# Optimization experiments

Measured on AMD Instinct MI355X. Metric: run time of the kernel, lower is better.

## Reference

```python
import jax, jax.numpy as jnp
import numpy as np

K, D = 512, 256
NUM_CLASSES, SHARED_KEYS = 10, 10
B, H, W = 32, 64, 64
TRAINING = True


def setup_inputs() -> dict:
    key = jax.random.key(0)
    k1, k2, k3 = jax.random.split(key, 3)
    z_e_x = jax.random.normal(k1, (B, D, H, W), dtype=jnp.float32)
    labels = jax.random.randint(k2, (B,), 0, NUM_CLASSES)
    # nn.Embedding weight initialized uniform(-1/K, 1/K)
    codebook = jax.random.uniform(k3, (K, D), minval=-1.0 / K, maxval=1.0 / K,
                                  dtype=jnp.float32)
    return {"z_e_x": z_e_x, "codebook": codebook, "labels": labels}


def _irrelevant_regions(labels_flat, k, num_classes, n_shared, training):
    # uniform partition of the first K - n_shared codes over the classes
    uniform = jnp.round(jnp.linspace(-0.5, num_classes - 0.51, k - n_shared))  # [K-Ns]
    irrel = uniform[None, :] != labels_flat[:, None].astype(uniform.dtype)     # [N, K-Ns]
    n = labels_flat.shape[0]
    if training:
        tail = jnp.ones((n, n_shared), dtype=bool)   # TRAIN: shared keys masked out
    else:
        tail = jnp.zeros((n, n_shared), dtype=bool)
    return jnp.concatenate([irrel, tail], axis=1)    # [N, K]


def reference(z_e_x, codebook, labels):
    x = jnp.transpose(z_e_x, (0, 2, 3, 1))           # [B,H,W,D]
    xf = x.reshape(-1, D)                            # [N,D], N=B*H*W
    labels_flat = jnp.repeat(labels, H * W)          # [N]

    irrel = _irrelevant_regions(labels_flat, K, NUM_CLASSES, SHARED_KEYS, TRAINING)

    cb_sqr = jnp.sum(codebook * codebook, axis=1)                      # [K]
    in_sqr = jnp.sum(xf * xf, axis=1, keepdims=True)                   # [N,1]
    distances = in_sqr + cb_sqr[None, :] - 2.0 * (xf @ codebook.T)     # [N,K]
    distances = jnp.where(irrel, jnp.inf, distances)

    idx = jnp.argmin(distances, axis=1)                                # [N]

    codes = codebook[idx].reshape(x.shape)                             # [B,H,W,D]
    # straight-through path (detached codebook in torch)
    z_q = x + jax.lax.stop_gradient(codes - x)
    z_q_x = jnp.transpose(z_q, (0, 3, 1, 2))                           # [B,D,H,W]
    # non-detached codebook lookup path
    z_q_bar = codebook[jax.lax.stop_gradient(idx)].reshape(x.shape)
    z_q_x_bar = jnp.transpose(z_q_bar, (0, 3, 1, 2))                   # [B,D,H,W]
    return (z_q_x, z_q_x_bar)
```

## Files before the change

### kernel.cpp

```cpp
#include <hip/hip_runtime.h>


#define D       256
#define KCODES  512
#define HW      4096
#define BATCH   32
#define NPTS    (BATCH * HW)
#define WPW     13
#define PF      8

typedef float fx4 __attribute__((ext_vector_type(4)));

__constant__ int c_cls_start[11] = {0, 51, 101, 151, 201, 251, 301, 352, 402, 452, 502};

__global__ __launch_bounds__(256) void prep_kernel(const float* __restrict__ cb,
                                                   float* __restrict__ cbT,
                                                   float* __restrict__ cbs) {
    const int k = blockIdx.x;
    const int d = threadIdx.x;
    float v = cb[k * D + d];
    cbT[(size_t)d * KCODES + k] = v;
    __shared__ double red[256];
    red[d] = (double)v * (double)v;
    __syncthreads();
    for (int s = 128; s > 0; s >>= 1) {
        if (d < s) red[d] += red[d + s];
        __syncthreads();
    }
    if (d == 0) cbs[k] = (float)red[0];
}

__global__ __launch_bounds__(256, 8) void argmin_kernel(const float* __restrict__ z,
                                                        const int* __restrict__ labels,
                                                        const float* __restrict__ cbT,
                                                        const float* __restrict__ cbs,
                                                        int* __restrict__ fidxg) {
    const int lane = threadIdx.x & 63;
    const int w    = __builtin_amdgcn_readfirstlane(threadIdx.x >> 6);
    const int b    = blockIdx.x >> 6;
    const int hw   = ((blockIdx.x & 63) << 6) | lane;
    const int lab  = __builtin_amdgcn_readfirstlane(labels[b]);
    const int c0   = c_cls_start[lab];
    const int cnt  = c_cls_start[lab + 1] - c0;
    const int kbase = c0 + w * WPW;
    const int myn   = min(WPW, cnt - w * WPW);

    const float* __restrict__ xp = z + (size_t)b * (D * HW) + hw;

    float acc[WPW];
#pragma unroll
    for (int j = 0; j < WPW; ++j) acc[j] = 0.0f;

    double xsq = 0.0;

    float xb[PF];
#pragma unroll
    for (int i = 0; i < PF; ++i) xb[i] = xp[(size_t)i * HW];

    for (int d = 0; d < D; d += PF) {
        float xn[PF];
#pragma unroll
        for (int i = 0; i < PF; ++i) {
            int dn = (d + PF + i) & (D - 1);
            xn[i] = xp[(size_t)dn * HW];
        }
#pragma unroll
        for (int i = 0; i < PF; ++i) {
            const float* __restrict__ wd = cbT + (size_t)(d + i) * KCODES + kbase;
            const float x = xb[i];
            xsq = fma((double)x, (double)x, xsq);
#pragma unroll
            for (int j = 0; j < WPW; ++j)
                acc[j] = fmaf(x, wd[j], acc[j]);
        }
#pragma unroll
        for (int i = 0; i < PF; ++i) xb[i] = xn[i];
    }

    const float insq = (float)xsq;
    float best = __builtin_inff();
    int bi = kbase;
#pragma unroll
    for (int j = 0; j < WPW; ++j) {
        if (j < myn) {
            float T    = insq + cbs[kbase + j];
            float dist = fmaf(-2.0f, acc[j], T);
            if (dist < best) { best = dist; bi = kbase + j; }
        }
    }

    __shared__ float sd[4][64];
    __shared__ int   si[4][64];
    sd[w][lane] = best;
    si[w][lane] = bi;
    __syncthreads();
    if (w == 0) {
        float fb = sd[0][lane];
        int   fi = si[0][lane];
#pragma unroll
        for (int w2 = 1; w2 < 4; ++w2) {
            float dv = sd[w2][lane];
            if (dv < fb) { fb = dv; fi = si[w2][lane]; }
        }
        fidxg[(size_t)b * HW + hw] = fi;
    }
}

__global__ __launch_bounds__(256) void emit_kernel(const int* __restrict__ fidxg,
                                                   const float* __restrict__ cbT,
                                                   float* __restrict__ out) {
    const int lane = threadIdx.x & 63;
    const int w    = threadIdx.x >> 6;
    const int s    = blockIdx.x >> 2;
    const int dq   = blockIdx.x & 3;
    const int b    = s >> 4;
    const int p0   = ((s & 15) << 8) | (lane << 2);

    const int4 f = *(const int4*)(fidxg + (size_t)b * HW + p0);

    float* __restrict__ o0 = out + (size_t)b * (D * HW) + p0;
    float* __restrict__ o1 = o0 + (size_t)NPTS * D;
    const int d0 = (dq << 6) | (w << 4);
    const float* __restrict__ row = cbT + (size_t)d0 * KCODES;
#pragma unroll 4
    for (int d = d0; d < d0 + 16; ++d) {
        fx4 v;
        v.x = row[f.x];
        v.y = row[f.y];
        v.z = row[f.z];
        v.w = row[f.w];
        __builtin_nontemporal_store(v, (fx4*)(o0 + (size_t)d * HW));
        __builtin_nontemporal_store(v, (fx4*)(o1 + (size_t)d * HW));
        row += KCODES;
    }
}

extern "C" void kernel_launch(void* const* d_in, const int* in_sizes, int n_in,
                              void* d_out, int out_size, void* d_ws, size_t ws_size,
                              hipStream_t stream) {
    const float* z      = (const float*)d_in[0];
    const float* cb     = (const float*)d_in[1];
    const int*   labels = (const int*)d_in[2];
    float* out = (float*)d_out;

    float* cbT  = (float*)d_ws;
    float* cbs  = cbT + (size_t)D * KCODES;
    int*   fidx = (int*)(cbs + KCODES);

    hipLaunchKernelGGL(prep_kernel, dim3(KCODES), dim3(D), 0, stream, cb, cbT, cbs);
    hipLaunchKernelGGL(argmin_kernel, dim3(NPTS / 64), dim3(256), 0, stream,
                       z, labels, cbT, cbs, fidx);
    hipLaunchKernelGGL(emit_kernel, dim3((NPTS / 256) * 4), dim3(256), 0, stream,
                       fidx, cbT, out);
}
```

Measured before the change: 393.7 us.

## Stage codebook chunks in per-wave double-buffered LDS for the distance loop

The argmin kernel now copies 32-row chunks of the transposed codebook slice for each wave's codes into a per-wave, double-buffered shared-memory tile, using register prefetch two chunks ahead. The inner FMA loop then reads codebook values from LDS instead of issuing wave-uniform global loads. The aim is to hide codebook fetch latency behind compute. The trade-offs are that the previously scalar, constant-cache-friendly uniform loads become LDS broadcast reads, and the kernel now needs 16KB of shared memory per block, which may limit occupancy.

```diff
diff --git a/kernel.cpp b/kernel.cpp
--- a/kernel.cpp
+++ b/kernel.cpp
@@ -8,6 +8,9 @@
 #define NPTS    (BATCH * HW)
 #define WPW     13
 #define PF      8
+#define CHUNK   32
+#define NCH     (D / CHUNK)
+#define SITER   8
 
 typedef float fx4 __attribute__((ext_vector_type(4)));
 
@@ -47,11 +50,36 @@
 
     const float* __restrict__ xp = z + (size_t)b * (D * HW) + hw;
 
+    __shared__ float cbl[4][2][CHUNK][16];
+
+    float sreg[SITER];
+    auto SLOAD = [&](int c) {
+        const float* __restrict__ base = cbT + (size_t)(c * CHUNK) * KCODES + kbase;
+#pragma unroll
+        for (int i = 0; i < SITER; ++i) {
+            int e = i * 64 + lane;
+            int j = e & 15;
+            if (j < WPW) sreg[i] = base[(size_t)(e >> 4) * KCODES + j];
+        }
+    };
+    auto SWRITE = [&](int buf) {
+        float* __restrict__ dst = &cbl[w][buf][0][0];
+#pragma unroll
+        for (int i = 0; i < SITER; ++i) {
+            int e = i * 64 + lane;
+            if ((e & 15) < WPW) dst[e] = sreg[i];
+        }
+    };
+
     float acc[WPW];
 #pragma unroll
     for (int j = 0; j < WPW; ++j) acc[j] = 0.0f;
 
     double xsq = 0.0;
+
+    SLOAD(0);
+    SWRITE(0);
+    SLOAD(1);
 
     float xb[PF];
 #pragma unroll
@@ -64,9 +92,16 @@
             int dn = (d + PF + i) & (D - 1);
             xn[i] = xp[(size_t)dn * HW];
         }
+        if ((d & (CHUNK - 1)) == CHUNK / 2) {
+            const int c = d >> 5;
+            if (c + 1 < NCH) SWRITE((c + 1) & 1);
+            if (c + 2 < NCH) SLOAD(c + 2);
+        }
+        const float* __restrict__ cur = &cbl[w][(d >> 5) & 1][0][0];
 #pragma unroll
         for (int i = 0; i < PF; ++i) {
-            const float* __restrict__ wd = cbT + (size_t)(d + i) * KCODES + kbase;
+            const int dl = (d & (CHUNK - 1)) + i;
+            const float* __restrict__ wd = cur + dl * 16;
             const float x = xb[i];
             xsq = fma((double)x, (double)x, xsq);
 #pragma unroll
```

Measured after the change: 436.8 us. 1.11x slower.
